# Kernel optimization log

Measured on AMD Instinct MI355X. Metric: run time of the kernel, lower is better.

The kernel has to match this reference:

```python
import jax, jax.numpy as jnp
import numpy as np

N_NODES = 100000
N_EDGES = 1600000
IN_F, HID, N_CLS = 512, 64, 32


def gcn_conv(x, edge_index, W, b, num_nodes):
    """PyG GCNConv: h = D^{-1/2} (A+I) D^{-1/2} (x W) + b."""
    loop = jnp.arange(num_nodes)
    src = jnp.concatenate([edge_index[0], loop])  # [E+N]
    dst = jnp.concatenate([edge_index[1], loop])
    # degree of target nodes (incl. self-loops)
    deg = jax.ops.segment_sum(jnp.ones_like(dst, dtype=x.dtype), dst,
                              num_segments=num_nodes)
    dinv = jnp.where(deg > 0, jax.lax.rsqrt(deg), 0.0)
    norm = dinv[src] * dinv[dst]  # [E+N]
    h = x @ W  # dense transform first (matches PyG: small out dim)
    msgs = h[src] * norm[:, None]  # edge-wise gather + scale
    out = jax.ops.segment_sum(msgs, dst, num_segments=num_nodes)  # scatter-add
    return out + b


def setup_inputs() -> dict:
    key = jax.random.key(0)
    k1, k2, k3, k4, k5, k6 = jax.random.split(key, 6)
    x = jax.random.normal(k1, (N_NODES, IN_F), dtype=jnp.float32)
    edge_index = jax.random.randint(k2, (2, N_EDGES), 0, N_NODES, dtype=jnp.int64)
    # Glorot-style init for the two GCNConv weights + biases
    W1 = jax.random.normal(k3, (IN_F, HID), dtype=jnp.float32) / np.sqrt(IN_F)
    b1 = jnp.zeros((HID,), dtype=jnp.float32)
    W2 = jax.random.normal(k4, (HID, N_CLS), dtype=jnp.float32) / np.sqrt(HID)
    b2 = jnp.zeros((N_CLS,), dtype=jnp.float32)
    return {"x": x, "edge_index": edge_index, "W1": W1, "b1": b1,
            "W2": W2, "b2": b2}


def reference(x, edge_index, W1, b1, W2, b2):
    num_nodes = x.shape[0]
    h = jax.nn.relu(gcn_conv(x, edge_index, W1, b1, num_nodes))
    z = gcn_conv(h, edge_index, W2, b2, num_nodes)
    return (h, z)
```

## Files before the change

kernel.cpp:

```cpp
#include <hip/hip_runtime.h>

#define N_NODES 100000
#define N_EDGES 1600000
#define IN_F 512
#define HID 64
#define N_CLS 32
#define NBKT2 391
#define EBLK 8192
#define NBLKA ((N_EDGES + EBLK - 1) / EBLK)

typedef __attribute__((ext_vector_type(8))) short short8;
typedef __attribute__((ext_vector_type(4))) float f32x4;

__device__ __forceinline__ unsigned short f2bf(float f) {
  unsigned int u = __float_as_uint(f);
  u += 0x7FFFu + ((u >> 16) & 1u);
  return (unsigned short)(u >> 16);
}
__device__ __forceinline__ float bf2f(unsigned int s) {
  return __uint_as_float(s << 16);
}

__global__ __launch_bounds__(256) void w1t_k(const float* __restrict__ W1,
                                             unsigned short* __restrict__ W1t,
                                             int* __restrict__ bcnt) {
  int i = blockIdx.x * 256 + threadIdx.x;
  if (i < NBKT2) bcnt[i] = 0;
  if (i < IN_F * HID) {
    int n = i >> 9, k = i & 511;
    W1t[i] = f2bf(W1[(size_t)k * HID + n]);
  }
}

__global__ __launch_bounds__(256) void coarse_hist_k(const int* __restrict__ ei,
                                                     int* __restrict__ bcnt,
                                                     int* __restrict__ bhist) {
  __shared__ int lh[NBKT2];
  int tid = threadIdx.x;
  for (int b = tid; b < NBKT2; b += 256) lh[b] = 0;
  __syncthreads();
  int e0 = blockIdx.x * EBLK;
  int e1 = min(e0 + EBLK, N_EDGES);
  for (int e = e0 + tid; e < e1; e += 256)
    atomicAdd(&lh[ei[N_EDGES + e] >> 8], 1);
  __syncthreads();
  for (int b = tid; b < NBKT2; b += 256) {
    int c = lh[b];
    bhist[blockIdx.x * NBKT2 + b] = c;
    if (c) atomicAdd(&bcnt[b], c);
  }
}

__global__ __launch_bounds__(512) void coarse_scan_k(const int* __restrict__ bcnt,
                                                     int* __restrict__ bbase,
                                                     int* __restrict__ bcur) {
  __shared__ int sc[512];
  int tid = threadIdx.x;
  int v = (tid < NBKT2) ? bcnt[tid] : 0;
  sc[tid] = v;
  __syncthreads();
  for (int off = 1; off < 512; off <<= 1) {
    int t = (tid >= off) ? sc[tid - off] : 0;
    __syncthreads();
    sc[tid] += t;
    __syncthreads();
  }
  int incl = sc[tid];
  int excl = incl - v;
  if (tid < NBKT2) { bbase[tid] = excl; bcur[tid] = excl; }
  if (tid == NBKT2 - 1) bbase[NBKT2] = incl;
}

__global__ __launch_bounds__(256) void passA_k(const int* __restrict__ ei,
                                               const int* __restrict__ bhist,
                                               int* __restrict__ bcur,
                                               unsigned* __restrict__ tmp) {
  __shared__ int gcur[NBKT2];
  int tid = threadIdx.x;
  int e0 = blockIdx.x * EBLK;
  int e1 = min(e0 + EBLK, N_EDGES);
  for (int b = tid; b < NBKT2; b += 256) {
    int c = bhist[blockIdx.x * NBKT2 + b];
    gcur[b] = c ? atomicAdd(&bcur[b], c) : 0;
  }
  __syncthreads();
  for (int e = e0 + tid; e < e1; e += 256) {
    int s = ei[e], d = ei[N_EDGES + e];
    int p = atomicAdd(&gcur[d >> 8], 1);
    tmp[p] = ((unsigned)s << 8) | (unsigned)(d & 255);
  }
}

__global__ __launch_bounds__(256) void passB_k(const unsigned* __restrict__ tmp,
                                               const int* __restrict__ bbase,
                                               int* __restrict__ rowptr,
                                               float* __restrict__ dinv,
                                               int* __restrict__ srcs) {
  __shared__ int sc[256];
  __shared__ int cur[256];
  int b = blockIdx.x, tid = threadIdx.x;
  int n0 = b << 8;
  int n1 = min(n0 + 256, N_NODES);
  int base = bbase[b], end = bbase[b + 1];
  sc[tid] = 0;
  __syncthreads();
  for (int i = base + tid; i < end; i += 256)
    atomicAdd(&sc[tmp[i] & 255u], 1);
  __syncthreads();
  int myc = sc[tid];
  for (int off = 1; off < 256; off <<= 1) {
    int t = (tid >= off) ? sc[tid - off] : 0;
    __syncthreads();
    sc[tid] += t;
    __syncthreads();
  }
  int incl = sc[tid];
  int excl = incl - myc;
  if (n0 + tid < n1) {
    rowptr[n0 + tid + 1] = base + incl;
    dinv[n0 + tid] = rsqrtf((float)(myc + 1));
  }
  if (b == 0 && tid == 0) rowptr[0] = 0;
  cur[tid] = base + excl;
  __syncthreads();
  for (int i = base + tid; i < end; i += 256) {
    unsigned v = tmp[i];
    int p = atomicAdd(&cur[v & 255u], 1);
    srcs[p] = (int)(v >> 8);
  }
}

__global__ __launch_bounds__(256) void gemm1_mfma_k(const float* __restrict__ x,
                                                    const unsigned short* __restrict__ W1t,
                                                    const float* __restrict__ dinv,
                                                    unsigned short* __restrict__ h0s) {
  __shared__ __align__(16) char As[64 * 128];
  __shared__ __align__(16) char Ws[64 * 128];
  int tid = threadIdx.x;
  int wave = tid >> 6, lane = tid & 63;
  int row0 = blockIdx.x * 64;
  f32x4 acc[4] = {{0.f,0.f,0.f,0.f},{0.f,0.f,0.f,0.f},{0.f,0.f,0.f,0.f},{0.f,0.f,0.f,0.f}};

  int l15 = lane & 15, lhi = lane >> 4;
  int rA = (wave << 4) + l15;

  for (int k0 = 0; k0 < IN_F; k0 += 64) {
    #pragma unroll
    for (int i = 0; i < 4; ++i) {
      int f = tid + i * 256;
      int r = f >> 4, c4 = (f & 15) << 2;
      float4 v = make_float4(0.f, 0.f, 0.f, 0.f);
      int gr = row0 + r;
      if (gr < N_NODES) v = *(const float4*)(x + (size_t)gr * IN_F + k0 + c4);
      ushort4 u;
      u.x = f2bf(v.x); u.y = f2bf(v.y); u.z = f2bf(v.z); u.w = f2bf(v.w);
      int byte = r * 128 + (c4 << 1);
      byte ^= (r & 7) << 4;
      *(ushort4*)(As + byte) = u;
    }
    #pragma unroll
    for (int i = 0; i < 2; ++i) {
      int f = tid + i * 256;
      int n = f >> 3, k8 = (f & 7) << 3;
      uint4 v = *(const uint4*)(W1t + (size_t)n * IN_F + k0 + k8);
      int byte = n * 128 + (k8 << 1);
      byte ^= (n & 7) << 4;
      *(uint4*)(Ws + byte) = v;
    }
    __syncthreads();
    #pragma unroll
    for (int ks = 0; ks < 64; ks += 32) {
      int kk = ks + (lhi << 3);
      int ba = rA * 128 + (kk << 1); ba ^= (rA & 7) << 4;
      short8 a = *(const short8*)(As + ba);
      #pragma unroll
      for (int j = 0; j < 4; ++j) {
        int nB = (j << 4) + l15;
        int bb = nB * 128 + (kk << 1); bb ^= (nB & 7) << 4;
        short8 bv = *(const short8*)(Ws + bb);
        acc[j] = __builtin_amdgcn_mfma_f32_16x16x32_bf16(a, bv, acc[j], 0, 0, 0);
      }
    }
    __syncthreads();
  }
  int rbase = row0 + (wave << 4) + (lhi << 2);
  #pragma unroll
  for (int r = 0; r < 4; ++r) {
    int gr = rbase + r;
    if (gr < N_NODES) {
      float dn = dinv[gr];
      #pragma unroll
      for (int j = 0; j < 4; ++j)
        h0s[(size_t)gr * HID + (j << 4) + l15] = f2bf(dn * acc[j][r]);
    }
  }
}

__global__ __launch_bounds__(256) void agg1g2_k(const uint4* __restrict__ h0q,
                                                const int* __restrict__ rowptr,
                                                const int* __restrict__ srcs,
                                                const float* __restrict__ dinv,
                                                const float* __restrict__ b1,
                                                const float* __restrict__ W2,
                                                float* __restrict__ out_h,
                                                unsigned short* __restrict__ h2b) {
  __shared__ float w2s[HID * N_CLS];
  __shared__ float hrow[4][HID];
  int tid = threadIdx.x;
  for (int i = tid; i < HID * N_CLS; i += 256) w2s[i] = W2[i];
  __syncthreads();

  int idx = blockIdx.x * 256 + tid;
  int node = idx >> 6;
  int wv = tid >> 6;
  int lane = tid & 63;
  int fl = lane & 7, g = lane >> 3;
  int p0 = rowptr[node], p1 = rowptr[node + 1];
  int c = p1 - p0;
  int ps = p0 + ((c * g) >> 3);
  int pe = p0 + ((c * (g + 1)) >> 3);
  float a[8] = {0.f,0.f,0.f,0.f,0.f,0.f,0.f,0.f};
  if (g == 0) {
    uint4 u = h0q[(size_t)node * 8 + fl];
    a[0] = bf2f(u.x & 0xffffu); a[1] = bf2f(u.x >> 16);
    a[2] = bf2f(u.y & 0xffffu); a[3] = bf2f(u.y >> 16);
    a[4] = bf2f(u.z & 0xffffu); a[5] = bf2f(u.z >> 16);
    a[6] = bf2f(u.w & 0xffffu); a[7] = bf2f(u.w >> 16);
  }
  int p = ps;
  for (; p + 2 <= pe; p += 2) {
    int s0 = srcs[p], s1 = srcs[p + 1];
    uint4 u0 = h0q[(size_t)s0 * 8 + fl];
    uint4 u1 = h0q[(size_t)s1 * 8 + fl];
    a[0] += bf2f(u0.x & 0xffffu) + bf2f(u1.x & 0xffffu);
    a[1] += bf2f(u0.x >> 16)     + bf2f(u1.x >> 16);
    a[2] += bf2f(u0.y & 0xffffu) + bf2f(u1.y & 0xffffu);
    a[3] += bf2f(u0.y >> 16)     + bf2f(u1.y >> 16);
    a[4] += bf2f(u0.z & 0xffffu) + bf2f(u1.z & 0xffffu);
    a[5] += bf2f(u0.z >> 16)     + bf2f(u1.z >> 16);
    a[6] += bf2f(u0.w & 0xffffu) + bf2f(u1.w & 0xffffu);
    a[7] += bf2f(u0.w >> 16)     + bf2f(u1.w >> 16);
  }
  if (p < pe) {
    uint4 u = h0q[(size_t)srcs[p] * 8 + fl];
    a[0] += bf2f(u.x & 0xffffu); a[1] += bf2f(u.x >> 16);
    a[2] += bf2f(u.y & 0xffffu); a[3] += bf2f(u.y >> 16);
    a[4] += bf2f(u.z & 0xffffu); a[5] += bf2f(u.z >> 16);
    a[6] += bf2f(u.w & 0xffffu); a[7] += bf2f(u.w >> 16);
  }
  #pragma unroll
  for (int off = 8; off < 64; off <<= 1) {
    #pragma unroll
    for (int i = 0; i < 8; ++i) a[i] += __shfl_xor(a[i], off);
  }
  float dn = dinv[node];
  if (g == 0) {
    float4 bA = *(const float4*)(b1 + fl * 8);
    float4 bB = *(const float4*)(b1 + fl * 8 + 4);
    float4 s0, s1;
    s0.x = fmaxf(dn * a[0] + bA.x, 0.f); s0.y = fmaxf(dn * a[1] + bA.y, 0.f);
    s0.z = fmaxf(dn * a[2] + bA.z, 0.f); s0.w = fmaxf(dn * a[3] + bA.w, 0.f);
    s1.x = fmaxf(dn * a[4] + bB.x, 0.f); s1.y = fmaxf(dn * a[5] + bB.y, 0.f);
    s1.z = fmaxf(dn * a[6] + bB.z, 0.f); s1.w = fmaxf(dn * a[7] + bB.w, 0.f);
    *(float4*)(out_h + (size_t)node * HID + fl * 8) = s0;
    *(float4*)(out_h + (size_t)node * HID + fl * 8 + 4) = s1;
    *(float4*)&hrow[wv][fl * 8] = s0;
    *(float4*)&hrow[wv][fl * 8 + 4] = s1;
  }
  int cls = lane & 31, kb = (lane >> 5) << 5;
  float acc2 = 0.f;
  #pragma unroll
  for (int k = 0; k < 32; ++k)
    acc2 += hrow[wv][kb + k] * w2s[(kb + k) * N_CLS + cls];
  acc2 += __shfl_xor(acc2, 32);
  if (lane < 32)
    h2b[(size_t)node * N_CLS + cls] = f2bf(dn * acc2);
}

__global__ __launch_bounds__(256) void agg2_k(const uint2* __restrict__ h2u,
                                              const int* __restrict__ rowptr,
                                              const int* __restrict__ srcs,
                                              const float* __restrict__ dinv,
                                              const float* __restrict__ b2,
                                              float* __restrict__ out) {
  int idx = blockIdx.x * 256 + threadIdx.x;
  int node = idx >> 6;
  if (node >= N_NODES) return;
  int lane = threadIdx.x & 63;
  int fl = lane & 7, g = lane >> 3;
  int p0 = rowptr[node], p1 = rowptr[node + 1];
  int c = p1 - p0;
  int ps = p0 + ((c * g) >> 3);
  int pe = p0 + ((c * (g + 1)) >> 3);
  float a0 = 0.f, a1 = 0.f, a2 = 0.f, a3 = 0.f;
  if (g == 0) {
    uint2 u = h2u[(size_t)node * 8 + fl];
    a0 = bf2f(u.x & 0xffffu); a1 = bf2f(u.x >> 16);
    a2 = bf2f(u.y & 0xffffu); a3 = bf2f(u.y >> 16);
  }
  int p = ps;
  for (; p + 2 <= pe; p += 2) {
    int s0 = srcs[p], s1 = srcs[p + 1];
    uint2 u0 = h2u[(size_t)s0 * 8 + fl];
    uint2 u1 = h2u[(size_t)s1 * 8 + fl];
    a0 += bf2f(u0.x & 0xffffu) + bf2f(u1.x & 0xffffu);
    a1 += bf2f(u0.x >> 16)     + bf2f(u1.x >> 16);
    a2 += bf2f(u0.y & 0xffffu) + bf2f(u1.y & 0xffffu);
    a3 += bf2f(u0.y >> 16)     + bf2f(u1.y >> 16);
  }
  if (p < pe) {
    uint2 u = h2u[(size_t)srcs[p] * 8 + fl];
    a0 += bf2f(u.x & 0xffffu); a1 += bf2f(u.x >> 16);
    a2 += bf2f(u.y & 0xffffu); a3 += bf2f(u.y >> 16);
  }
  #pragma unroll
  for (int off = 8; off < 64; off <<= 1) {
    a0 += __shfl_xor(a0, off); a1 += __shfl_xor(a1, off);
    a2 += __shfl_xor(a2, off); a3 += __shfl_xor(a3, off);
  }
  if (g == 0) {
    float dn = dinv[node];
    float4 bv = *(const float4*)(b2 + fl * 4);
    float4 st;
    st.x = dn * a0 + bv.x; st.y = dn * a1 + bv.y;
    st.z = dn * a2 + bv.z; st.w = dn * a3 + bv.w;
    *(float4*)(out + (size_t)node * N_CLS + fl * 4) = st;
  }
}

extern "C" void kernel_launch(void* const* d_in, const int* in_sizes, int n_in,
                              void* d_out, int out_size, void* d_ws, size_t ws_size,
                              hipStream_t stream) {
  const float* x  = (const float*)d_in[0];
  const int*   ei = (const int*)d_in[1];
  const float* W1 = (const float*)d_in[2];
  const float* b1 = (const float*)d_in[3];
  const float* W2 = (const float*)d_in[4];
  const float* b2 = (const float*)d_in[5];
  float* out_h = (float*)d_out;
  float* out_z = out_h + (size_t)N_NODES * HID;

  char* ws = (char*)d_ws;
  int* bcnt           = (int*)(ws + 0);
  int* bbase          = (int*)(ws + (4 << 10));
  int* bcur           = (int*)(ws + (8 << 10));
  int* bhist          = (int*)(ws + (12 << 10));
  int* rowptr         = (int*)(ws + (336 << 10));
  float* dinv         = (float*)(ws + (752 << 10));
  unsigned short* W1t = (unsigned short*)(ws + (1168 << 10));
  unsigned* tmp       = (unsigned*)(ws + (1280 << 10));
  int* srcs           = (int*)(ws + (8ull << 20));
  unsigned short* h0s = (unsigned short*)(ws + (15ull << 20));
  unsigned short* h2b = (unsigned short*)(ws + (28ull << 20));

  w1t_k<<<(IN_F * HID + 255) / 256, 256, 0, stream>>>(W1, W1t, bcnt);
  coarse_hist_k<<<NBLKA, 256, 0, stream>>>(ei, bcnt, bhist);
  coarse_scan_k<<<1, 512, 0, stream>>>(bcnt, bbase, bcur);
  passA_k<<<NBLKA, 256, 0, stream>>>(ei, bhist, bcur, tmp);
  passB_k<<<NBKT2, 256, 0, stream>>>(tmp, bbase, rowptr, dinv, srcs);
  gemm1_mfma_k<<<(N_NODES + 63) / 64, 256, 0, stream>>>(x, W1t, dinv, h0s);
  agg1g2_k<<<(N_NODES * 64) / 256, 256, 0, stream>>>((const uint4*)h0s, rowptr, srcs,
                                                     dinv, b1, W2, out_h, h2b);
  agg2_k<<<(N_NODES * 64) / 256, 256, 0, stream>>>((const uint2*)h2b, rowptr, srcs,
                                                   dinv, b2, out_z);
}
```

Baseline: 217.2 us.

## Split histogram finer, widen CSR build blocks, use 16B gathers in agg2

The coarse histogram now runs over four times as many smaller edge blocks, and passA sums four sub-histograms per block. passA and passB move to 512-thread blocks. Index loads in both aggregation kernels become nontemporal. agg2 switches to 16-byte row loads with 16 edge groups per node instead of 8. Together these aim to add parallelism to the CSR construction and make the gathers more efficient, at the cost of a larger histogram workspace and more shuffle-reduction steps.

```diff
diff --git a/kernel.cpp b/kernel.cpp
--- a/kernel.cpp
+++ b/kernel.cpp
@@ -8,6 +8,8 @@
 #define NBKT2 391
 #define EBLK 8192
 #define NBLKA ((N_EDGES + EBLK - 1) / EBLK)
+#define EBLKH 2048
+#define NBLKH (NBLKA * 4)
 
 typedef __attribute__((ext_vector_type(8))) short short8;
 typedef __attribute__((ext_vector_type(4))) float f32x4;
@@ -39,8 +41,8 @@
   int tid = threadIdx.x;
   for (int b = tid; b < NBKT2; b += 256) lh[b] = 0;
   __syncthreads();
-  int e0 = blockIdx.x * EBLK;
-  int e1 = min(e0 + EBLK, N_EDGES);
+  int e0 = blockIdx.x * EBLKH;
+  int e1 = min(e0 + EBLKH, N_EDGES);
   for (int e = e0 + tid; e < e1; e += 256)
     atomicAdd(&lh[ei[N_EDGES + e] >> 8], 1);
   __syncthreads();
@@ -71,7 +73,7 @@
   if (tid == NBKT2 - 1) bbase[NBKT2] = incl;
 }
 
-__global__ __launch_bounds__(256) void passA_k(const int* __restrict__ ei,
+__global__ __launch_bounds__(512) void passA_k(const int* __restrict__ ei,
                                                const int* __restrict__ bhist,
                                                int* __restrict__ bcur,
                                                unsigned* __restrict__ tmp) {
@@ -79,19 +81,21 @@
   int tid = threadIdx.x;
   int e0 = blockIdx.x * EBLK;
   int e1 = min(e0 + EBLK, N_EDGES);
-  for (int b = tid; b < NBKT2; b += 256) {
-    int c = bhist[blockIdx.x * NBKT2 + b];
+  int rb = (blockIdx.x * 4) * NBKT2;
+  for (int b = tid; b < NBKT2; b += 512) {
+    int c = bhist[rb + b] + bhist[rb + NBKT2 + b] +
+            bhist[rb + 2 * NBKT2 + b] + bhist[rb + 3 * NBKT2 + b];
     gcur[b] = c ? atomicAdd(&bcur[b], c) : 0;
   }
   __syncthreads();
-  for (int e = e0 + tid; e < e1; e += 256) {
+  for (int e = e0 + tid; e < e1; e += 512) {
     int s = ei[e], d = ei[N_EDGES + e];
     int p = atomicAdd(&gcur[d >> 8], 1);
     tmp[p] = ((unsigned)s << 8) | (unsigned)(d & 255);
   }
 }
 
-__global__ __launch_bounds__(256) void passB_k(const unsigned* __restrict__ tmp,
+__global__ __launch_bounds__(512) void passB_k(const unsigned* __restrict__ tmp,
                                                const int* __restrict__ bbase,
                                                int* __restrict__ rowptr,
                                                float* __restrict__ dinv,
@@ -102,28 +106,30 @@
   int n0 = b << 8;
   int n1 = min(n0 + 256, N_NODES);
   int base = bbase[b], end = bbase[b + 1];
-  sc[tid] = 0;
-  __syncthreads();
-  for (int i = base + tid; i < end; i += 256)
+  if (tid < 256) sc[tid] = 0;
+  __syncthreads();
+  for (int i = base + tid; i < end; i += 512)
     atomicAdd(&sc[tmp[i] & 255u], 1);
   __syncthreads();
-  int myc = sc[tid];
+  int myc = (tid < 256) ? sc[tid] : 0;
   for (int off = 1; off < 256; off <<= 1) {
-    int t = (tid >= off) ? sc[tid - off] : 0;
-    __syncthreads();
-    sc[tid] += t;
-    __syncthreads();
-  }
-  int incl = sc[tid];
-  int excl = incl - myc;
-  if (n0 + tid < n1) {
-    rowptr[n0 + tid + 1] = base + incl;
-    dinv[n0 + tid] = rsqrtf((float)(myc + 1));
+    int t = (tid < 256 && tid >= off) ? sc[tid - off] : 0;
+    __syncthreads();
+    if (tid < 256) sc[tid] += t;
+    __syncthreads();
+  }
+  if (tid < 256) {
+    int incl = sc[tid];
+    int excl = incl - myc;
+    if (n0 + tid < n1) {
+      rowptr[n0 + tid + 1] = base + incl;
+      dinv[n0 + tid] = rsqrtf((float)(myc + 1));
+    }
+    cur[tid] = base + excl;
   }
   if (b == 0 && tid == 0) rowptr[0] = 0;
-  cur[tid] = base + excl;
-  __syncthreads();
-  for (int i = base + tid; i < end; i += 256) {
+  __syncthreads();
+  for (int i = base + tid; i < end; i += 512) {
     unsigned v = tmp[i];
     int p = atomicAdd(&cur[v & 255u], 1);
     srcs[p] = (int)(v >> 8);
@@ -229,7 +235,8 @@
   }
   int p = ps;
   for (; p + 2 <= pe; p += 2) {
-    int s0 = srcs[p], s1 = srcs[p + 1];
+    int s0 = __builtin_nontemporal_load(srcs + p);
+    int s1 = __builtin_nontemporal_load(srcs + p + 1);
     uint4 u0 = h0q[(size_t)s0 * 8 + fl];
     uint4 u1 = h0q[(size_t)s1 * 8 + fl];
     a[0] += bf2f(u0.x & 0xffffu) + bf2f(u1.x & 0xffffu);
@@ -242,7 +249,8 @@
     a[7] += bf2f(u0.w >> 16)     + bf2f(u1.w >> 16);
   }
   if (p < pe) {
-    uint4 u = h0q[(size_t)srcs[p] * 8 + fl];
+    int s0 = __builtin_nontemporal_load(srcs + p);
+    uint4 u = h0q[(size_t)s0 * 8 + fl];
     a[0] += bf2f(u.x & 0xffffu); a[1] += bf2f(u.x >> 16);
     a[2] += bf2f(u.y & 0xffffu); a[3] += bf2f(u.y >> 16);
     a[4] += bf2f(u.z & 0xffffu); a[5] += bf2f(u.z >> 16);
@@ -277,7 +285,7 @@
     h2b[(size_t)node * N_CLS + cls] = f2bf(dn * acc2);
 }
 
-__global__ __launch_bounds__(256) void agg2_k(const uint2* __restrict__ h2u,
+__global__ __launch_bounds__(256) void agg2_k(const uint4* __restrict__ h2q,
                                               const int* __restrict__ rowptr,
                                               const int* __restrict__ srcs,
                                               const float* __restrict__ dinv,
@@ -287,44 +295,58 @@
   int node = idx >> 6;
   if (node >= N_NODES) return;
   int lane = threadIdx.x & 63;
-  int fl = lane & 7, g = lane >> 3;
+  int fl = lane & 3, g = lane >> 2;
   int p0 = rowptr[node], p1 = rowptr[node + 1];
   int c = p1 - p0;
-  int ps = p0 + ((c * g) >> 3);
-  int pe = p0 + ((c * (g + 1)) >> 3);
-  float a0 = 0.f, a1 = 0.f, a2 = 0.f, a3 = 0.f;
+  int ps = p0 + ((c * g) >> 4);
+  int pe = p0 + ((c * (g + 1)) >> 4);
+  float a[8] = {0.f,0.f,0.f,0.f,0.f,0.f,0.f,0.f};
   if (g == 0) {
-    uint2 u = h2u[(size_t)node * 8 + fl];
-    a0 = bf2f(u.x & 0xffffu); a1 = bf2f(u.x >> 16);
-    a2 = bf2f(u.y & 0xffffu); a3 = bf2f(u.y >> 16);
+    uint4 u = h2q[(size_t)node * 4 + fl];
+    a[0] = bf2f(u.x & 0xffffu); a[1] = bf2f(u.x >> 16);
+    a[2] = bf2f(u.y & 0xffffu); a[3] = bf2f(u.y >> 16);
+    a[4] = bf2f(u.z & 0xffffu); a[5] = bf2f(u.z >> 16);
+    a[6] = bf2f(u.w & 0xffffu); a[7] = bf2f(u.w >> 16);
   }
   int p = ps;
   for (; p + 2 <= pe; p += 2) {
-    int s0 = srcs[p], s1 = srcs[p + 1];
-    uint2 u0 = h2u[(size_t)s0 * 8 + fl];
-    uint2 u1 = h2u[(size_t)s1 * 8 + fl];
-    a0 += bf2f(u0.x & 0xffffu) + bf2f(u1.x & 0xffffu);
-    a1 += bf2f(u0.x >> 16)     + bf2f(u1.x >> 16);
-    a2 += bf2f(u0.y & 0xffffu) + bf2f(u1.y & 0xffffu);
-    a3 += bf2f(u0.y >> 16)     + bf2f(u1.y >> 16);
+    int s0 = __builtin_nontemporal_load(srcs + p);
+    int s1 = __builtin_nontemporal_load(srcs + p + 1);
+    uint4 u0 = h2q[(size_t)s0 * 4 + fl];
+    uint4 u1 = h2q[(size_t)s1 * 4 + fl];
+    a[0] += bf2f(u0.x & 0xffffu) + bf2f(u1.x & 0xffffu);
+    a[1] += bf2f(u0.x >> 16)     + bf2f(u1.x >> 16);
+    a[2] += bf2f(u0.y & 0xffffu) + bf2f(u1.y & 0xffffu);
+    a[3] += bf2f(u0.y >> 16)     + bf2f(u1.y >> 16);
+    a[4] += bf2f(u0.z & 0xffffu) + bf2f(u1.z & 0xffffu);
+    a[5] += bf2f(u0.z >> 16)     + bf2f(u1.z >> 16);
+    a[6] += bf2f(u0.w & 0xffffu) + bf2f(u1.w & 0xffffu);
+    a[7] += bf2f(u0.w >> 16)     + bf2f(u1.w >> 16);
   }
   if (p < pe) {
-    uint2 u = h2u[(size_t)srcs[p] * 8 + fl];
-    a0 += bf2f(u.x & 0xffffu); a1 += bf2f(u.x >> 16);
-    a2 += bf2f(u.y & 0xffffu); a3 += bf2f(u.y >> 16);
+    int s0 = __builtin_nontemporal_load(srcs + p);
+    uint4 u = h2q[(size_t)s0 * 4 + fl];
+    a[0] += bf2f(u.x & 0xffffu); a[1] += bf2f(u.x >> 16);
+    a[2] += bf2f(u.y & 0xffffu); a[3] += bf2f(u.y >> 16);
+    a[4] += bf2f(u.z & 0xffffu); a[5] += bf2f(u.z >> 16);
+    a[6] += bf2f(u.w & 0xffffu); a[7] += bf2f(u.w >> 16);
   }
   #pragma unroll
-  for (int off = 8; off < 64; off <<= 1) {
-    a0 += __shfl_xor(a0, off); a1 += __shfl_xor(a1, off);
-    a2 += __shfl_xor(a2, off); a3 += __shfl_xor(a3, off);
+  for (int off = 4; off < 64; off <<= 1) {
+    #pragma unroll
+    for (int i = 0; i < 8; ++i) a[i] += __shfl_xor(a[i], off);
   }
   if (g == 0) {
     float dn = dinv[node];
-    float4 bv = *(const float4*)(b2 + fl * 4);
-    float4 st;
-    st.x = dn * a0 + bv.x; st.y = dn * a1 + bv.y;
-    st.z = dn * a2 + bv.z; st.w = dn * a3 + bv.w;
-    *(float4*)(out + (size_t)node * N_CLS + fl * 4) = st;
+    float4 bA = *(const float4*)(b2 + fl * 8);
+    float4 bB = *(const float4*)(b2 + fl * 8 + 4);
+    float4 s0, s1;
+    s0.x = dn * a[0] + bA.x; s0.y = dn * a[1] + bA.y;
+    s0.z = dn * a[2] + bA.z; s0.w = dn * a[3] + bA.w;
+    s1.x = dn * a[4] + bB.x; s1.y = dn * a[5] + bB.y;
+    s1.z = dn * a[6] + bB.z; s1.w = dn * a[7] + bB.w;
+    *(float4*)(out + (size_t)node * N_CLS + fl * 8) = s0;
+    *(float4*)(out + (size_t)node * N_CLS + fl * 8 + 4) = s1;
   }
 }
 
@@ -344,23 +366,23 @@
   int* bcnt           = (int*)(ws + 0);
   int* bbase          = (int*)(ws + (4 << 10));
   int* bcur           = (int*)(ws + (8 << 10));
-  int* bhist          = (int*)(ws + (12 << 10));
-  int* rowptr         = (int*)(ws + (336 << 10));
-  float* dinv         = (float*)(ws + (752 << 10));
-  unsigned short* W1t = (unsigned short*)(ws + (1168 << 10));
-  unsigned* tmp       = (unsigned*)(ws + (1280 << 10));
-  int* srcs           = (int*)(ws + (8ull << 20));
-  unsigned short* h0s = (unsigned short*)(ws + (15ull << 20));
-  unsigned short* h2b = (unsigned short*)(ws + (28ull << 20));
+  int* bhist          = (int*)(ws + (16 << 10));
+  int* rowptr         = (int*)(ws + (1216 << 10));
+  float* dinv         = (float*)(ws + (1616 << 10));
+  unsigned short* W1t = (unsigned short*)(ws + (2016 << 10));
+  unsigned* tmp       = (unsigned*)(ws + (2112 << 10));
+  int* srcs           = (int*)(ws + (8448ull << 10));
+  unsigned short* h0s = (unsigned short*)(ws + (14720ull << 10));
+  unsigned short* h2b = (unsigned short*)(ws + (27264ull << 10));
 
   w1t_k<<<(IN_F * HID + 255) / 256, 256, 0, stream>>>(W1, W1t, bcnt);
-  coarse_hist_k<<<NBLKA, 256, 0, stream>>>(ei, bcnt, bhist);
+  coarse_hist_k<<<NBLKH, 256, 0, stream>>>(ei, bcnt, bhist);
   coarse_scan_k<<<1, 512, 0, stream>>>(bcnt, bbase, bcur);
-  passA_k<<<NBLKA, 256, 0, stream>>>(ei, bhist, bcur, tmp);
-  passB_k<<<NBKT2, 256, 0, stream>>>(tmp, bbase, rowptr, dinv, srcs);
+  passA_k<<<NBLKA, 512, 0, stream>>>(ei, bhist, bcur, tmp);
+  passB_k<<<NBKT2, 512, 0, stream>>>(tmp, bbase, rowptr, dinv, srcs);
   gemm1_mfma_k<<<(N_NODES + 63) / 64, 256, 0, stream>>>(x, W1t, dinv, h0s);
   agg1g2_k<<<(N_NODES * 64) / 256, 256, 0, stream>>>((const uint4*)h0s, rowptr, srcs,
                                                      dinv, b1, W2, out_h, h2b);
-  agg2_k<<<(N_NODES * 64) / 256, 256, 0, stream>>>((const uint2*)h2b, rowptr, srcs,
+  agg2_k<<<(N_NODES * 64) / 256, 256, 0, stream>>>((const uint4*)h2b, rowptr, srcs,
                                                    dinv, b2, out_z);
 }
```

After: 222.4 us. 1.02x slower.
